# Kernel tuning notes

Hardware: AMD Instinct MI355X
Metric: run time of the kernel (lower is better)

Reference implementation:

```python
import jax, jax.numpy as jnp
import numpy as np

B, A, H, L = 4096, 4096, 768, 4  # batch, num_atoms, hidden_dim, antecedent_len


def setup_inputs() -> dict:
    key = jax.random.key(0)
    ks = jax.random.split(key, 10)
    s = 0.02
    cls = jax.random.normal(ks[0], (B, H), jnp.float32)
    x_ = jax.random.bernoulli(ks[1], 0.5, (B, A)).astype(jnp.float32)
    gru_w_ih = jax.random.normal(ks[2], (3 * H, H), jnp.float32) * s
    gru_w_hh = jax.random.normal(ks[3], (3 * H, H), jnp.float32) * s
    gru_b_ih = jax.random.normal(ks[4], (3 * H,), jnp.float32) * s
    gru_b_hh = jax.random.normal(ks[5], (3 * H,), jnp.float32) * s
    head_w = jax.random.normal(ks[6], (A, H), jnp.float32) * s
    head_b = jax.random.normal(ks[7], (A,), jnp.float32) * s
    ae_weight = jax.random.normal(ks[8], (A, H), jnp.float32) * s
    return {"cls": cls, "x_": x_, "gru_w_ih": gru_w_ih, "gru_w_hh": gru_w_hh,
            "gru_b_ih": gru_b_ih, "gru_b_hh": gru_b_hh, "head_w": head_w,
            "head_b": head_b, "ae_weight": ae_weight}


def _gru_step(x, h, w_ih, w_hh, b_ih, b_hh):
    # torch GRU gate order: r, z, n
    gi = x @ w_ih.T + b_ih          # [B, 3H]
    gh = h @ w_hh.T + b_hh
    i_r, i_z, i_n = jnp.split(gi, 3, axis=-1)
    h_r, h_z, h_n = jnp.split(gh, 3, axis=-1)
    r = jax.nn.sigmoid(i_r + h_r)
    z = jax.nn.sigmoid(i_z + h_z)
    n = jnp.tanh(i_n + r * h_n)
    return (1.0 - z) * n + z * h


def reference(cls, x_, gru_w_ih, gru_w_hh, gru_b_ih, gru_b_hh, head_w, head_b, ae_weight):
    key = jax.random.key(42)
    mask = x_
    h = jnp.zeros_like(cls)
    cur_input = cls
    max_index = None
    rows = jnp.arange(B)
    probs = []
    for j in range(L):
        h = _gru_step(cur_input, h, gru_w_ih, gru_w_hh, gru_b_ih, gru_b_hh)
        out = h @ head_w.T + head_b  # [B, A]  (dropout = identity in eval)
        # filtered_softmax mask update (mutations persist across steps)
        if j == 0:
            empty = jnp.sum(mask, axis=-1) == 0.0
            mask = mask.at[:, 0].set(jnp.where(empty, 1.0, mask[:, 0]))
        else:
            mask = jnp.where((max_index == 0)[:, None], 0.0, mask)
            mask = mask.at[:, 0].set(1.0)
        logits = jnp.where(mask > 0, out, -jnp.inf)
        # hard gumbel-softmax, tau=1 (straight-through)
        key, sub = jax.random.split(key)
        g = jax.random.gumbel(sub, logits.shape, logits.dtype)
        y_soft = jax.nn.softmax(logits + g, axis=1)
        idx = jnp.argmax(y_soft, axis=1)
        y_hard = jax.nn.one_hot(idx, A, dtype=y_soft.dtype)
        prob = y_hard + y_soft - jax.lax.stop_gradient(y_soft)
        max_index = idx
        # scatter zeros at the selected atom (remove from candidate set)
        mask = mask.at[rows, idx].set(0.0)
        probs.append(prob)
        atom_wsum = prob @ jax.lax.stop_gradient(ae_weight)  # [B, H]
        cur_input = cls + atom_wsum
    return jnp.stack(probs, axis=1)  # [B, L, A]
```

## Files before the change

### kernel.cpp

```cpp
#include <hip/hip_runtime.h>
#include <cstdint>
#include <cstddef>
#include <math.h>


#define KB 4096
#define KA 4096
#define KH 768
#define KL 4

typedef __attribute__((ext_vector_type(8))) short bf16x8;
typedef __attribute__((ext_vector_type(4))) float f32x4;

__host__ __device__ inline unsigned rotl32(unsigned x, int d) {
  return (x << d) | (x >> (32 - d));
}

__host__ __device__ inline void tf2x32(unsigned k0, unsigned k1,
                                       unsigned x0, unsigned x1,
                                       unsigned& o0, unsigned& o1) {
  unsigned ks2 = k0 ^ k1 ^ 0x1BD11BDAu;
  x0 += k0; x1 += k1;
#define TF_R(r) { x0 += x1; x1 = rotl32(x1, (r)); x1 ^= x0; }
  TF_R(13) TF_R(15) TF_R(26) TF_R(6)
  x0 += k1;  x1 += ks2 + 1u;
  TF_R(17) TF_R(29) TF_R(16) TF_R(24)
  x0 += ks2; x1 += k0 + 2u;
  TF_R(13) TF_R(15) TF_R(26) TF_R(6)
  x0 += k0;  x1 += k1 + 3u;
  TF_R(17) TF_R(29) TF_R(16) TF_R(24)
  x0 += k1;  x1 += ks2 + 4u;
  TF_R(13) TF_R(15) TF_R(26) TF_R(6)
  x0 += ks2; x1 += k0 + 5u;
#undef TF_R
  o0 = x0; o1 = x1;
}

__device__ inline ushort f2bf(float f) {
  unsigned u = __float_as_uint(f);
  unsigned r = (u + 0x7fffu + ((u >> 16) & 1u)) >> 16;
  return (ushort)r;
}
__device__ inline float bf2f(ushort h) {
  return __uint_as_float(((unsigned)h) << 16);
}

__device__ inline float gumbel_at(unsigned s0, unsigned s1, unsigned ctr) {
  unsigned o0, o1;
  tf2x32(s0, s1, 0u, ctr, o0, o1);
  unsigned bits = o0 ^ o1;
  float f = __uint_as_float((bits >> 9) | 0x3f800000u) - 1.0f;
  const float TINY = 1.17549435e-38f;
  float u = fmaxf(TINY, f + TINY);
  return -logf(-logf(u));
}

#define GLDS(gp, lp) \
  __builtin_amdgcn_global_load_lds( \
      (const __attribute__((address_space(1))) void*)(gp), \
      (__attribute__((address_space(3))) void*)(lp), 16, 0, 0)

__global__ __launch_bounds__(256) void gemm3_nt(
    const ushort* __restrict__ Ahi, const ushort* __restrict__ Alo,
    const ushort* __restrict__ Bhi, const ushort* __restrict__ Blo,
    float* __restrict__ C, long long ldc) {
  __shared__ ushort smem[4 * 128 * 32];
  const int tid = threadIdx.x;
  const int wave = tid >> 6;
  const int lane = tid & 63;
  const long long bm = (long long)blockIdx.y * 128;
  const long long bn = (long long)blockIdx.x * 128;
  const int wm = (wave & 1) * 64;
  const int wn = (wave >> 1) * 64;

  f32x4 acc[4][4];
#pragma unroll
  for (int i = 0; i < 4; ++i)
#pragma unroll
    for (int j = 0; j < 4; ++j) acc[i][j] = (f32x4){0.f, 0.f, 0.f, 0.f};

  const int r = lane >> 2;
  const int cs = lane & 3;
  const int csrc = cs ^ ((r & 3) ^ ((r >> 2) & 3));
  const int m15 = lane & 15;
  const int kg = (lane >> 4) & 3;
  const int slot = kg ^ ((m15 & 3) ^ ((m15 >> 2) & 3));

  for (int kt = 0; kt < 24; ++kt) {
    const int k0 = kt * 32;
#pragma unroll
    for (int s = 0; s < 2; ++s) {
      const int m0 = wave * 32 + s * 16;
      const long long arow = (bm + m0 + r) * KH + k0 + csrc * 8;
      const long long brow = (bn + m0 + r) * KH + k0 + csrc * 8;
      GLDS(Ahi + arow, &smem[0 * 4096 + m0 * 32]);
      GLDS(Alo + arow, &smem[1 * 4096 + m0 * 32]);
      GLDS(Bhi + brow, &smem[2 * 4096 + m0 * 32]);
      GLDS(Blo + brow, &smem[3 * 4096 + m0 * 32]);
    }
    __syncthreads();
    bf16x8 bh[4], bl[4];
#pragma unroll
    for (int jj = 0; jj < 4; ++jj) {
      const int n = wn + jj * 16 + m15;
      bh[jj] = *(const bf16x8*)&smem[2 * 4096 + n * 32 + slot * 8];
      bl[jj] = *(const bf16x8*)&smem[3 * 4096 + n * 32 + slot * 8];
    }
#pragma unroll
    for (int i = 0; i < 4; ++i) {
      const int m = wm + i * 16 + m15;
      bf16x8 ah = *(const bf16x8*)&smem[0 * 4096 + m * 32 + slot * 8];
      bf16x8 al = *(const bf16x8*)&smem[1 * 4096 + m * 32 + slot * 8];
#pragma unroll
      for (int jj = 0; jj < 4; ++jj) {
        acc[i][jj] = __builtin_amdgcn_mfma_f32_16x16x32_bf16(ah, bh[jj], acc[i][jj], 0, 0, 0);
        acc[i][jj] = __builtin_amdgcn_mfma_f32_16x16x32_bf16(ah, bl[jj], acc[i][jj], 0, 0, 0);
        acc[i][jj] = __builtin_amdgcn_mfma_f32_16x16x32_bf16(al, bh[jj], acc[i][jj], 0, 0, 0);
      }
    }
    __syncthreads();
  }
  const int rq = (lane >> 4) * 4;
#pragma unroll
  for (int i = 0; i < 4; ++i)
#pragma unroll
    for (int j = 0; j < 4; ++j) {
      const long long n = bn + wn + j * 16 + m15;
#pragma unroll
      for (int rg = 0; rg < 4; ++rg) {
        const long long m = bm + wm + i * 16 + rq + rg;
        C[m * ldc + n] = acc[i][j][rg];
      }
    }
}

__global__ __launch_bounds__(256) void gemm1_nt(
    const ushort* __restrict__ Ahi, const ushort* __restrict__ Bhi,
    float* __restrict__ C, long long ldc) {
  __shared__ ushort smem[2 * 128 * 32];
  const int tid = threadIdx.x;
  const int wave = tid >> 6;
  const int lane = tid & 63;
  const long long bm = (long long)blockIdx.y * 128;
  const long long bn = (long long)blockIdx.x * 128;
  const int wm = (wave & 1) * 64;
  const int wn = (wave >> 1) * 64;

  f32x4 acc[4][4];
#pragma unroll
  for (int i = 0; i < 4; ++i)
#pragma unroll
    for (int j = 0; j < 4; ++j) acc[i][j] = (f32x4){0.f, 0.f, 0.f, 0.f};

  const int r = lane >> 2;
  const int cs = lane & 3;
  const int csrc = cs ^ ((r & 3) ^ ((r >> 2) & 3));
  const int m15 = lane & 15;
  const int kg = (lane >> 4) & 3;
  const int slot = kg ^ ((m15 & 3) ^ ((m15 >> 2) & 3));

  for (int kt = 0; kt < 24; ++kt) {
    const int k0 = kt * 32;
#pragma unroll
    for (int s = 0; s < 2; ++s) {
      const int m0 = wave * 32 + s * 16;
      const long long arow = (bm + m0 + r) * KH + k0 + csrc * 8;
      const long long brow = (bn + m0 + r) * KH + k0 + csrc * 8;
      GLDS(Ahi + arow, &smem[0 * 4096 + m0 * 32]);
      GLDS(Bhi + brow, &smem[1 * 4096 + m0 * 32]);
    }
    __syncthreads();
    bf16x8 bh[4];
#pragma unroll
    for (int jj = 0; jj < 4; ++jj) {
      const int n = wn + jj * 16 + m15;
      bh[jj] = *(const bf16x8*)&smem[1 * 4096 + n * 32 + slot * 8];
    }
#pragma unroll
    for (int i = 0; i < 4; ++i) {
      const int m = wm + i * 16 + m15;
      bf16x8 ah = *(const bf16x8*)&smem[0 * 4096 + m * 32 + slot * 8];
#pragma unroll
      for (int jj = 0; jj < 4; ++jj)
        acc[i][jj] = __builtin_amdgcn_mfma_f32_16x16x32_bf16(ah, bh[jj], acc[i][jj], 0, 0, 0);
    }
    __syncthreads();
  }
  const int rq = (lane >> 4) * 4;
#pragma unroll
  for (int i = 0; i < 4; ++i)
#pragma unroll
    for (int j = 0; j < 4; ++j) {
      const long long n = bn + wn + j * 16 + m15;
#pragma unroll
      for (int rg = 0; rg < 4; ++rg) {
        const long long m = bm + wm + i * 16 + rq + rg;
        C[m * ldc + n] = acc[i][j][rg];
      }
    }
}

#define CUM1 442368
#define CUM2 884736
#define CUM3 1671168
#define CUM4 2457600
#define CUM5 3244032
#define PREP_CONV_BLOCKS 12672

__global__ void prep(const float* __restrict__ w_ih, const float* __restrict__ w_hh,
                     const float* __restrict__ head_w, const float* __restrict__ cls,
                     const float* __restrict__ ae_w, const float* __restrict__ x_,
                     ushort* __restrict__ WihHi, ushort* __restrict__ WihLo,
                     ushort* __restrict__ WhhHi, ushort* __restrict__ WhhLo,
                     ushort* __restrict__ HwHi, ushort* __restrict__ CAhi,
                     ushort* __restrict__ CAlo, unsigned char* __restrict__ empty) {
  const int blk = blockIdx.x;
  const int tid = threadIdx.x;
  if (blk < PREP_CONV_BLOCKS) {
    const int i = blk * 256 + tid;
    const float* src; ushort* dhi; ushort* dlo; int base; int split; int ofs = 0;
    if (i < CUM1)      { src = w_ih;   dhi = WihHi; dlo = WihLo; base = 0;    split = 1; }
    else if (i < CUM2) { src = w_hh;   dhi = WhhHi; dlo = WhhLo; base = CUM1; split = 1; }
    else if (i < CUM3) { src = head_w; dhi = HwHi;  dlo = 0;     base = CUM2; split = 0; }
    else if (i < CUM4) { src = cls;    dhi = CAhi;  dlo = CAlo;  base = CUM3; split = 1; }
    else               { src = ae_w;   dhi = CAhi;  dlo = CAlo;  base = CUM4; split = 1; ofs = 786432; }
    const int k = i - base;
    float4 v = ((const float4*)src)[k];
    ushort4 h;
    h.x = f2bf(v.x); h.y = f2bf(v.y); h.z = f2bf(v.z); h.w = f2bf(v.w);
    ((ushort4*)dhi)[ofs + k] = h;
    if (split) {
      ushort4 l;
      l.x = f2bf(v.x - bf2f(h.x)); l.y = f2bf(v.y - bf2f(h.y));
      l.z = f2bf(v.z - bf2f(h.z)); l.w = f2bf(v.w - bf2f(h.w));
      ((ushort4*)dlo)[ofs + k] = l;
    }
  } else {
    const int row = blk - PREP_CONV_BLOCKS;
    __shared__ int scnt[256];
    const float4* xr = (const float4*)(x_ + (size_t)row * KA);
    int cnt = 0;
#pragma unroll
    for (int k = 0; k < 4; ++k) {
      float4 v = xr[tid + (k << 8)];
      cnt += (v.x != 0.f) + (v.y != 0.f) + (v.z != 0.f) + (v.w != 0.f);
    }
    scnt[tid] = cnt;
    __syncthreads();
    for (int s = 128; s > 0; s >>= 1) {
      if (tid < s) scnt[tid] += scnt[tid + s];
      __syncthreads();
    }
    if (tid == 0) empty[row] = (scnt[0] == 0) ? 1 : 0;
  }
}

__global__ void gru_gate2(const float* __restrict__ PAE, const float* __restrict__ Gh,
                          const int* __restrict__ idxbuf,
                          const float* __restrict__ b_ih, const float* __restrict__ b_hh,
                          float* __restrict__ h, ushort* __restrict__ hHi,
                          ushort* __restrict__ hLo, int first) {
  int i4 = blockIdx.x * 256 + threadIdx.x;
  int b = i4 / (KH / 4);
  int c4 = i4 - b * (KH / 4);
  const f32x4* gp = (const f32x4*)(PAE + (size_t)b * (3 * KH));
  f32x4 ir = gp[c4], iz = gp[c4 + 192], inn = gp[c4 + 384];
  const f32x4* bi = (const f32x4*)b_ih;
  const f32x4* bhh = (const f32x4*)b_hh;
  f32x4 hr = bhh[c4], hz = bhh[c4 + 192], hn = bhh[c4 + 384];
  f32x4 hp = (f32x4){0.f, 0.f, 0.f, 0.f};
  if (!first) {
    const f32x4* ga = (const f32x4*)(PAE + ((size_t)KB + idxbuf[b]) * (3 * KH));
    ir += ga[c4]; iz += ga[c4 + 192]; inn += ga[c4 + 384];
    const f32x4* gh = (const f32x4*)(Gh + (size_t)b * (3 * KH));
    hr += gh[c4]; hz += gh[c4 + 192]; hn += gh[c4 + 384];
    hp = ((const f32x4*)h)[i4];
  }
  ir += bi[c4]; iz += bi[c4 + 192]; inn += bi[c4 + 384];
  f32x4 hv;
  ushort4 hh, hl;
  ushort* hhp = &hh.x;
  ushort* hlp = &hl.x;
#pragma unroll
  for (int e = 0; e < 4; ++e) {
    float rr = 1.f / (1.f + expf(-(ir[e] + hr[e])));
    float z = 1.f / (1.f + expf(-(iz[e] + hz[e])));
    float n = tanhf(inn[e] + rr * hn[e]);
    float v = (1.f - z) * n + z * hp[e];
    hv[e] = v;
    ushort hb = f2bf(v);
    hhp[e] = hb;
    hlp[e] = f2bf(v - bf2f(hb));
  }
  ((f32x4*)h)[i4] = hv;
  ((ushort4*)hHi)[i4] = hh;
  ((ushort4*)hLo)[i4] = hl;
}

__global__ __launch_bounds__(256) void sample_step(
    float* __restrict__ out, const float* __restrict__ head_b,
    const float* __restrict__ x_, unsigned char* __restrict__ mask,
    int* __restrict__ idxbuf, const float* __restrict__ hbuf,
    const float* __restrict__ head_w, const unsigned char* __restrict__ empty,
    int j, unsigned s0, unsigned s1) {
  const int b = blockIdx.x;
  const int tid = threadIdx.x;
  float* orow = out + ((size_t)b * KL + j) * KA;
  unsigned char* mrow = mask + (size_t)b * KA;
  const float* xrow = x_ + (size_t)b * KA;
  __shared__ float sv[256];
  __shared__ int scand[16];
  __shared__ float srefined[16];
  __shared__ int scnt;
  __shared__ int ssel;
  const float EPS = 0.01f;

  if (tid == 0) scnt = 0;

  const int idx_prev = (j > 0) ? idxbuf[b] : 0;
  const int emp = (j == 0) ? empty[b] : 0;

  float vreg[16];
  unsigned mbits = 0;
  float lmax = -INFINITY;
  const float4* orow4 = (const float4*)orow;
  const float4* xrow4 = (const float4*)xrow;
  const unsigned* mrow4 = (const unsigned*)mrow;
  const float4* hb4 = (const float4*)head_b;
#pragma unroll
  for (int k = 0; k < 4; ++k) {
    const int ci = tid + (k << 8);
    const int abase = ci * 4;
    float4 lv = orow4[ci];
    float4 hbv = hb4[ci];
    float lvv[4] = {lv.x + hbv.x, lv.y + hbv.y, lv.z + hbv.z, lv.w + hbv.w};
    float xvv[4] = {0.f, 0.f, 0.f, 0.f};
    unsigned mword = 0;
    if (j == 0) {
      float4 xv = xrow4[ci];
      xvv[0] = xv.x; xvv[1] = xv.y; xvv[2] = xv.z; xvv[3] = xv.w;
    } else {
      mword = mrow4[ci];
    }
#pragma unroll
    for (int e = 0; e < 4; ++e) {
      const int a = abase + e;
      int m;
      if (j == 0) {
        m = (xvv[e] != 0.f) || (emp && a == 0);
      } else {
        m = (a == 0) || (idx_prev != 0 && ((mword >> (8 * e)) & 0xffu));
      }
      float v = -INFINITY;
      if (m) {
        float g = gumbel_at(s0, s1, (unsigned)(b * KA + a));
        v = lvv[e] + g;
        mbits |= (1u << (k * 4 + e));
      }
      vreg[k * 4 + e] = v;
      lmax = fmaxf(lmax, v);
    }
  }
  sv[tid] = lmax;
  __syncthreads();
  for (int s = 128; s > 0; s >>= 1) {
    if (tid < s) sv[tid] = fmaxf(sv[tid], sv[tid + s]);
    __syncthreads();
  }
  const float vmax = sv[0];

  const float thresh = vmax - EPS;
#pragma unroll
  for (int k = 0; k < 4; ++k)
#pragma unroll
    for (int e = 0; e < 4; ++e) {
      if (vreg[k * 4 + e] >= thresh) {
        int slot = atomicAdd(&scnt, 1);
        if (slot < 16) scand[slot] = (tid + (k << 8)) * 4 + e;
      }
    }
  __syncthreads();
  const int ncand = min(scnt, 16);

  {
    const int wv = tid >> 6;
    const int lane = tid & 63;
    const float4* h4 = (const float4*)(hbuf + (size_t)b * KH);
    for (int t = wv; t < ncand; t += 4) {
      const int a = scand[t];
      const float4* w4 = (const float4*)(head_w + (size_t)a * KH);
      float sum = 0.f;
#pragma unroll
      for (int u = 0; u < 3; ++u) {
        float4 hv = h4[lane + u * 64];
        float4 wv4 = w4[lane + u * 64];
        sum = fmaf(hv.x, wv4.x, sum);
        sum = fmaf(hv.y, wv4.y, sum);
        sum = fmaf(hv.z, wv4.z, sum);
        sum = fmaf(hv.w, wv4.w, sum);
      }
#pragma unroll
      for (int off = 32; off > 0; off >>= 1) sum += __shfl_down(sum, off);
      if (lane == 0) {
        float g = gumbel_at(s0, s1, (unsigned)(b * KA + a));
        srefined[t] = sum + head_b[a] + g;
      }
    }
  }
  __syncthreads();

  if (tid == 0) {
    float best = -INFINITY;
    int bsel = KA;
    for (int t = 0; t < ncand; ++t) {
      float v = srefined[t];
      int a = scand[t];
      if (v > best || (v == best && a < bsel)) { best = v; bsel = a; }
    }
    ssel = bsel;
  }
  __syncthreads();
  const int sel = ssel;

#pragma unroll
  for (int k = 0; k < 4; ++k) {
    const int ci = tid + (k << 8);
    const int abase = ci * 4;
    unsigned mw = 0;
    float4 ov;
    float* ovp = &ov.x;
#pragma unroll
    for (int e = 0; e < 4; ++e) {
      const int a = abase + e;
      int m = (mbits >> (k * 4 + e)) & 1;
      if (a == sel) m = 0;
      mw |= ((unsigned)m) << (8 * e);
      ovp[e] = (a == sel) ? 1.f : 0.f;
    }
    ((unsigned*)mrow)[ci] = mw;
    ((float4*)orow)[ci] = ov;
  }
  if (tid == 0) idxbuf[b] = sel;
}

extern "C" void kernel_launch(void* const* d_in, const int* in_sizes, int n_in,
                              void* d_out, int out_size, void* d_ws, size_t ws_size,
                              hipStream_t stream) {
  const float* cls    = (const float*)d_in[0];
  const float* x_     = (const float*)d_in[1];
  const float* w_ih   = (const float*)d_in[2];
  const float* w_hh   = (const float*)d_in[3];
  const float* b_ih   = (const float*)d_in[4];
  const float* b_hh   = (const float*)d_in[5];
  const float* head_w = (const float*)d_in[6];
  const float* head_b = (const float*)d_in[7];
  const float* ae_w   = (const float*)d_in[8];
  float* out = (float*)d_out;

  char* p = (char*)d_ws;
  ushort* CAhi  = (ushort*)p; p += (size_t)2 * KB * KH * 2;
  ushort* CAlo  = (ushort*)p; p += (size_t)2 * KB * KH * 2;
  ushort* WihHi = (ushort*)p; p += (size_t)3 * KH * KH * 2;
  ushort* WihLo = (ushort*)p; p += (size_t)3 * KH * KH * 2;
  ushort* WhhHi = (ushort*)p; p += (size_t)3 * KH * KH * 2;
  ushort* WhhLo = (ushort*)p; p += (size_t)3 * KH * KH * 2;
  ushort* HwHi  = (ushort*)p; p += (size_t)KA * KH * 2;
  ushort* hHi   = (ushort*)p; p += (size_t)KB * KH * 2;
  ushort* hLo   = (ushort*)p; p += (size_t)KB * KH * 2;
  float*  hbuf  = (float*)p;  p += (size_t)KB * KH * 4;
  float*  PAE   = (float*)p;  p += (size_t)2 * KB * 3 * KH * 4;
  float*  Gh    = (float*)p;  p += (size_t)KB * 3 * KH * 4;
  unsigned char* mask  = (unsigned char*)p; p += (size_t)KB * KA;
  unsigned char* empty = (unsigned char*)p; p += (size_t)KB;
  int* idxbuf = (int*)p; p += (size_t)KB * 4;

  unsigned key0 = 0u, key1 = 42u;
  unsigned sub0[KL], sub1[KL];
  for (int j = 0; j < KL; ++j) {
    unsigned n0, n1, t0, t1;
    tf2x32(key0, key1, 0u, 0u, n0, n1);
    tf2x32(key0, key1, 0u, 1u, t0, t1);
    sub0[j] = t0; sub1[j] = t1;
    key0 = n0; key1 = n1;
  }

  prep<<<PREP_CONV_BLOCKS + KB, 256, 0, stream>>>(
      w_ih, w_hh, head_w, cls, ae_w, x_,
      WihHi, WihLo, WhhHi, WhhLo, HwHi, CAhi, CAlo, empty);
  gemm3_nt<<<dim3(3 * KH / 128, 2 * KB / 128), 256, 0, stream>>>(
      CAhi, CAlo, WihHi, WihLo, PAE, 3 * KH);

  for (int j = 0; j < KL; ++j) {
    if (j > 0)
      gemm3_nt<<<dim3(3 * KH / 128, KB / 128), 256, 0, stream>>>(
          hHi, hLo, WhhHi, WhhLo, Gh, 3 * KH);
    gru_gate2<<<KB * KH / 4 / 256, 256, 0, stream>>>(PAE, Gh, idxbuf, b_ih, b_hh,
                                                     hbuf, hHi, hLo, j == 0);
    gemm1_nt<<<dim3(KA / 128, KB / 128), 256, 0, stream>>>(
        hHi, HwHi, out + (size_t)j * KA, (long long)KL * KA);
    sample_step<<<KB, 256, 0, stream>>>(out, head_b, x_, mask, idxbuf, hbuf,
                                        head_w, empty, j, sub0[j], sub1[j]);
  }
}
```

Measured before the change: 1.055 ms.

## Fuse next-step Whh GEMM with head GEMM and store bf16 logits

The recurrent Whh GEMM for the next step is merged with the head projection GEMM into one launch, with blocks split by index, because both depend only on the current h. The head GEMM now adds head_b and writes bf16 logits to a separate buffer instead of fp32 into the output. The sampler reads this buffer, 8 elements per vector load. Storing in bf16 is why the candidate-refinement epsilon widens from 0.01 to 0.02; a narrow window risks missing the true argmax when more than 16 candidates fall inside it.

```diff
diff --git a/kernel.cpp b/kernel.cpp
--- a/kernel.cpp
+++ b/kernel.cpp
@@ -134,24 +134,18 @@
     }
 }
 
-__global__ __launch_bounds__(256) void gemm1_nt(
-    const ushort* __restrict__ Ahi, const ushort* __restrict__ Bhi,
-    float* __restrict__ C, long long ldc) {
-  __shared__ ushort smem[2 * 128 * 32];
+__global__ __launch_bounds__(256) void gemm_fused(
+    const ushort* __restrict__ hHi, const ushort* __restrict__ hLo,
+    const ushort* __restrict__ WhhHi, const ushort* __restrict__ WhhLo,
+    float* __restrict__ Gh, const ushort* __restrict__ HwHi,
+    const float* __restrict__ head_b, ushort* __restrict__ Vbuf, int gh_nb) {
+  __shared__ ushort smem[4 * 128 * 32];
   const int tid = threadIdx.x;
   const int wave = tid >> 6;
   const int lane = tid & 63;
-  const long long bm = (long long)blockIdx.y * 128;
-  const long long bn = (long long)blockIdx.x * 128;
+  const int bid = blockIdx.x;
   const int wm = (wave & 1) * 64;
   const int wn = (wave >> 1) * 64;
-
-  f32x4 acc[4][4];
-#pragma unroll
-  for (int i = 0; i < 4; ++i)
-#pragma unroll
-    for (int j = 0; j < 4; ++j) acc[i][j] = (f32x4){0.f, 0.f, 0.f, 0.f};
-
   const int r = lane >> 2;
   const int cs = lane & 3;
   const int csrc = cs ^ ((r & 3) ^ ((r >> 2) & 3));
@@ -159,45 +153,106 @@
   const int kg = (lane >> 4) & 3;
   const int slot = kg ^ ((m15 & 3) ^ ((m15 >> 2) & 3));
 
-  for (int kt = 0; kt < 24; ++kt) {
-    const int k0 = kt * 32;
-#pragma unroll
-    for (int s = 0; s < 2; ++s) {
-      const int m0 = wave * 32 + s * 16;
-      const long long arow = (bm + m0 + r) * KH + k0 + csrc * 8;
-      const long long brow = (bn + m0 + r) * KH + k0 + csrc * 8;
-      GLDS(Ahi + arow, &smem[0 * 4096 + m0 * 32]);
-      GLDS(Bhi + brow, &smem[1 * 4096 + m0 * 32]);
-    }
-    __syncthreads();
-    bf16x8 bh[4];
-#pragma unroll
-    for (int jj = 0; jj < 4; ++jj) {
-      const int n = wn + jj * 16 + m15;
-      bh[jj] = *(const bf16x8*)&smem[1 * 4096 + n * 32 + slot * 8];
-    }
-#pragma unroll
-    for (int i = 0; i < 4; ++i) {
-      const int m = wm + i * 16 + m15;
-      bf16x8 ah = *(const bf16x8*)&smem[0 * 4096 + m * 32 + slot * 8];
-#pragma unroll
-      for (int jj = 0; jj < 4; ++jj)
-        acc[i][jj] = __builtin_amdgcn_mfma_f32_16x16x32_bf16(ah, bh[jj], acc[i][jj], 0, 0, 0);
-    }
-    __syncthreads();
-  }
-  const int rq = (lane >> 4) * 4;
+  f32x4 acc[4][4];
 #pragma unroll
   for (int i = 0; i < 4; ++i)
 #pragma unroll
-    for (int j = 0; j < 4; ++j) {
-      const long long n = bn + wn + j * 16 + m15;
-#pragma unroll
-      for (int rg = 0; rg < 4; ++rg) {
-        const long long m = bm + wm + i * 16 + rq + rg;
-        C[m * ldc + n] = acc[i][j][rg];
-      }
-    }
+    for (int j = 0; j < 4; ++j) acc[i][j] = (f32x4){0.f, 0.f, 0.f, 0.f};
+
+  if (bid < gh_nb) {
+    const long long bm = (long long)(bid / 18) * 128;
+    const long long bn = (long long)(bid % 18) * 128;
+    for (int kt = 0; kt < 24; ++kt) {
+      const int k0 = kt * 32;
+#pragma unroll
+      for (int s = 0; s < 2; ++s) {
+        const int m0 = wave * 32 + s * 16;
+        const long long arow = (bm + m0 + r) * KH + k0 + csrc * 8;
+        const long long brow = (bn + m0 + r) * KH + k0 + csrc * 8;
+        GLDS(hHi + arow, &smem[0 * 4096 + m0 * 32]);
+        GLDS(hLo + arow, &smem[1 * 4096 + m0 * 32]);
+        GLDS(WhhHi + brow, &smem[2 * 4096 + m0 * 32]);
+        GLDS(WhhLo + brow, &smem[3 * 4096 + m0 * 32]);
+      }
+      __syncthreads();
+      bf16x8 bh[4], bl[4];
+#pragma unroll
+      for (int jj = 0; jj < 4; ++jj) {
+        const int n = wn + jj * 16 + m15;
+        bh[jj] = *(const bf16x8*)&smem[2 * 4096 + n * 32 + slot * 8];
+        bl[jj] = *(const bf16x8*)&smem[3 * 4096 + n * 32 + slot * 8];
+      }
+#pragma unroll
+      for (int i = 0; i < 4; ++i) {
+        const int m = wm + i * 16 + m15;
+        bf16x8 ah = *(const bf16x8*)&smem[0 * 4096 + m * 32 + slot * 8];
+        bf16x8 al = *(const bf16x8*)&smem[1 * 4096 + m * 32 + slot * 8];
+#pragma unroll
+        for (int jj = 0; jj < 4; ++jj) {
+          acc[i][jj] = __builtin_amdgcn_mfma_f32_16x16x32_bf16(ah, bh[jj], acc[i][jj], 0, 0, 0);
+          acc[i][jj] = __builtin_amdgcn_mfma_f32_16x16x32_bf16(ah, bl[jj], acc[i][jj], 0, 0, 0);
+          acc[i][jj] = __builtin_amdgcn_mfma_f32_16x16x32_bf16(al, bh[jj], acc[i][jj], 0, 0, 0);
+        }
+      }
+      __syncthreads();
+    }
+    const int rq = (lane >> 4) * 4;
+#pragma unroll
+    for (int i = 0; i < 4; ++i)
+#pragma unroll
+      for (int j = 0; j < 4; ++j) {
+        const long long n = bn + wn + j * 16 + m15;
+#pragma unroll
+        for (int rg = 0; rg < 4; ++rg) {
+          const long long m = bm + wm + i * 16 + rq + rg;
+          Gh[m * (3 * KH) + n] = acc[i][j][rg];
+        }
+      }
+  } else {
+    const int k = bid - gh_nb;
+    const long long bm = (long long)(k >> 5) * 128;
+    const long long bn = (long long)(k & 31) * 128;
+    for (int kt = 0; kt < 24; ++kt) {
+      const int k0 = kt * 32;
+#pragma unroll
+      for (int s = 0; s < 2; ++s) {
+        const int m0 = wave * 32 + s * 16;
+        const long long arow = (bm + m0 + r) * KH + k0 + csrc * 8;
+        const long long brow = (bn + m0 + r) * KH + k0 + csrc * 8;
+        GLDS(hHi + arow, &smem[0 * 4096 + m0 * 32]);
+        GLDS(HwHi + brow, &smem[1 * 4096 + m0 * 32]);
+      }
+      __syncthreads();
+      bf16x8 bh[4];
+#pragma unroll
+      for (int jj = 0; jj < 4; ++jj) {
+        const int n = wn + jj * 16 + m15;
+        bh[jj] = *(const bf16x8*)&smem[1 * 4096 + n * 32 + slot * 8];
+      }
+#pragma unroll
+      for (int i = 0; i < 4; ++i) {
+        const int m = wm + i * 16 + m15;
+        bf16x8 ah = *(const bf16x8*)&smem[0 * 4096 + m * 32 + slot * 8];
+#pragma unroll
+        for (int jj = 0; jj < 4; ++jj)
+          acc[i][jj] = __builtin_amdgcn_mfma_f32_16x16x32_bf16(ah, bh[jj], acc[i][jj], 0, 0, 0);
+      }
+      __syncthreads();
+    }
+    const int rq = (lane >> 4) * 4;
+#pragma unroll
+    for (int i = 0; i < 4; ++i)
+#pragma unroll
+      for (int j = 0; j < 4; ++j) {
+        const long long n = bn + wn + j * 16 + m15;
+        const float hb = head_b[n];
+#pragma unroll
+        for (int rg = 0; rg < 4; ++rg) {
+          const long long m = bm + wm + i * 16 + rq + rg;
+          Vbuf[m * KA + n] = f2bf(acc[i][j][rg] + hb);
+        }
+      }
+  }
 }
 
 #define CUM1 442368
@@ -298,22 +353,23 @@
 }
 
 __global__ __launch_bounds__(256) void sample_step(
-    float* __restrict__ out, const float* __restrict__ head_b,
+    float* __restrict__ out, const ushort* __restrict__ Vbuf,
     const float* __restrict__ x_, unsigned char* __restrict__ mask,
     int* __restrict__ idxbuf, const float* __restrict__ hbuf,
-    const float* __restrict__ head_w, const unsigned char* __restrict__ empty,
-    int j, unsigned s0, unsigned s1) {
+    const float* __restrict__ head_w, const float* __restrict__ head_b,
+    const unsigned char* __restrict__ empty, int j, unsigned s0, unsigned s1) {
   const int b = blockIdx.x;
   const int tid = threadIdx.x;
   float* orow = out + ((size_t)b * KL + j) * KA;
   unsigned char* mrow = mask + (size_t)b * KA;
-  const float* xrow = x_ + (size_t)b * KA;
+  const ushort* vrow = Vbuf + (size_t)b * KA;
+  const float4* xrow4 = (const float4*)(x_ + (size_t)b * KA);
   __shared__ float sv[256];
   __shared__ int scand[16];
   __shared__ float srefined[16];
   __shared__ int scnt;
   __shared__ int ssel;
-  const float EPS = 0.01f;
+  const float EPS = 0.02f;
 
   if (tid == 0) scnt = 0;
 
@@ -323,41 +379,41 @@
   float vreg[16];
   unsigned mbits = 0;
   float lmax = -INFINITY;
-  const float4* orow4 = (const float4*)orow;
-  const float4* xrow4 = (const float4*)xrow;
-  const unsigned* mrow4 = (const unsigned*)mrow;
-  const float4* hb4 = (const float4*)head_b;
-#pragma unroll
-  for (int k = 0; k < 4; ++k) {
+#pragma unroll
+  for (int k = 0; k < 2; ++k) {
     const int ci = tid + (k << 8);
-    const int abase = ci * 4;
-    float4 lv = orow4[ci];
-    float4 hbv = hb4[ci];
-    float lvv[4] = {lv.x + hbv.x, lv.y + hbv.y, lv.z + hbv.z, lv.w + hbv.w};
-    float xvv[4] = {0.f, 0.f, 0.f, 0.f};
-    unsigned mword = 0;
+    const int abase = ci * 8;
+    uint4 vv = ((const uint4*)vrow)[ci];
+    unsigned vw[4] = {vv.x, vv.y, vv.z, vv.w};
+    float xv[8];
+    unsigned mw0 = 0, mw1 = 0;
     if (j == 0) {
-      float4 xv = xrow4[ci];
-      xvv[0] = xv.x; xvv[1] = xv.y; xvv[2] = xv.z; xvv[3] = xv.w;
+      float4 x0 = xrow4[ci * 2], x1 = xrow4[ci * 2 + 1];
+      xv[0] = x0.x; xv[1] = x0.y; xv[2] = x0.z; xv[3] = x0.w;
+      xv[4] = x1.x; xv[5] = x1.y; xv[6] = x1.z; xv[7] = x1.w;
     } else {
-      mword = mrow4[ci];
-    }
-#pragma unroll
-    for (int e = 0; e < 4; ++e) {
+      uint2 mwv = ((const uint2*)mrow)[ci];
+      mw0 = mwv.x; mw1 = mwv.y;
+    }
+#pragma unroll
+    for (int e = 0; e < 8; ++e) {
       const int a = abase + e;
       int m;
       if (j == 0) {
-        m = (xvv[e] != 0.f) || (emp && a == 0);
+        m = (xv[e] != 0.f) || (emp && a == 0);
       } else {
-        m = (a == 0) || (idx_prev != 0 && ((mword >> (8 * e)) & 0xffu));
+        unsigned mb = (e < 4) ? ((mw0 >> (8 * e)) & 0xffu)
+                              : ((mw1 >> (8 * (e - 4))) & 0xffu);
+        m = (a == 0) || (idx_prev != 0 && mb);
       }
       float v = -INFINITY;
       if (m) {
+        ushort hv16 = (ushort)((vw[e >> 1] >> (16 * (e & 1))) & 0xffffu);
         float g = gumbel_at(s0, s1, (unsigned)(b * KA + a));
-        v = lvv[e] + g;
-        mbits |= (1u << (k * 4 + e));
-      }
-      vreg[k * 4 + e] = v;
+        v = bf2f(hv16) + g;
+        mbits |= (1u << (k * 8 + e));
+      }
+      vreg[k * 8 + e] = v;
       lmax = fmaxf(lmax, v);
     }
   }
@@ -371,12 +427,12 @@
 
   const float thresh = vmax - EPS;
 #pragma unroll
-  for (int k = 0; k < 4; ++k)
-#pragma unroll
-    for (int e = 0; e < 4; ++e) {
-      if (vreg[k * 4 + e] >= thresh) {
+  for (int k = 0; k < 2; ++k)
+#pragma unroll
+    for (int e = 0; e < 8; ++e) {
+      if (vreg[k * 8 + e] >= thresh) {
         int slot = atomicAdd(&scnt, 1);
-        if (slot < 16) scand[slot] = (tid + (k << 8)) * 4 + e;
+        if (slot < 16) scand[slot] = (tid + (k << 8)) * 8 + e;
       }
     }
   __syncthreads();
@@ -423,22 +479,22 @@
   const int sel = ssel;
 
 #pragma unroll
-  for (int k = 0; k < 4; ++k) {
+  for (int k = 0; k < 2; ++k) {
     const int ci = tid + (k << 8);
-    const int abase = ci * 4;
-    unsigned mw = 0;
-    float4 ov;
-    float* ovp = &ov.x;
-#pragma unroll
-    for (int e = 0; e < 4; ++e) {
+    const int abase = ci * 8;
+    unsigned mw[2] = {0u, 0u};
+    float ov[8];
+#pragma unroll
+    for (int e = 0; e < 8; ++e) {
       const int a = abase + e;
-      int m = (mbits >> (k * 4 + e)) & 1;
+      int m = (mbits >> (k * 8 + e)) & 1;
       if (a == sel) m = 0;
-      mw |= ((unsigned)m) << (8 * e);
-      ovp[e] = (a == sel) ? 1.f : 0.f;
-    }
-    ((unsigned*)mrow)[ci] = mw;
-    ((float4*)orow)[ci] = ov;
+      mw[e >> 2] |= ((unsigned)m) << (8 * (e & 3));
+      ov[e] = (a == sel) ? 1.f : 0.f;
+    }
+    ((uint2*)mrow)[ci] = make_uint2(mw[0], mw[1]);
+    ((float4*)orow)[ci * 2]     = make_float4(ov[0], ov[1], ov[2], ov[3]);
+    ((float4*)orow)[ci * 2 + 1] = make_float4(ov[4], ov[5], ov[6], ov[7]);
   }
   if (tid == 0) idxbuf[b] = sel;
 }
@@ -470,6 +526,7 @@
   float*  hbuf  = (float*)p;  p += (size_t)KB * KH * 4;
   float*  PAE   = (float*)p;  p += (size_t)2 * KB * 3 * KH * 4;
   float*  Gh    = (float*)p;  p += (size_t)KB * 3 * KH * 4;
+  ushort* Vbuf  = (ushort*)p; p += (size_t)KB * KA * 2;
   unsigned char* mask  = (unsigned char*)p; p += (size_t)KB * KA;
   unsigned char* empty = (unsigned char*)p; p += (size_t)KB;
   int* idxbuf = (int*)p; p += (size_t)KB * 4;
@@ -491,14 +548,12 @@
       CAhi, CAlo, WihHi, WihLo, PAE, 3 * KH);
 
   for (int j = 0; j < KL; ++j) {
-    if (j > 0)
-      gemm3_nt<<<dim3(3 * KH / 128, KB / 128), 256, 0, stream>>>(
-          hHi, hLo, WhhHi, WhhLo, Gh, 3 * KH);
     gru_gate2<<<KB * KH / 4 / 256, 256, 0, stream>>>(PAE, Gh, idxbuf, b_ih, b_hh,
                                                      hbuf, hHi, hLo, j == 0);
-    gemm1_nt<<<dim3(KA / 128, KB / 128), 256, 0, stream>>>(
-        hHi, HwHi, out + (size_t)j * KA, (long long)KL * KA);
-    sample_step<<<KB, 256, 0, stream>>>(out, head_b, x_, mask, idxbuf, hbuf,
-                                        head_w, empty, j, sub0[j], sub1[j]);
-  }
-}
+    const int gh_nb = (j < KL - 1) ? 576 : 0;
+    gemm_fused<<<gh_nb + 1024, 256, 0, stream>>>(
+        hHi, hLo, WhhHi, WhhLo, Gh, HwHi, head_b, Vbuf, gh_nb);
+    sample_step<<<KB, 256, 0, stream>>>(out, Vbuf, x_, mask, idxbuf, hbuf,
+                                        head_w, head_b, empty, j, sub0[j], sub1[j]);
+  }
+}
```

Result: faster. 1.029 ms (-2.4%).
